# Performance work log

Measured on AMD Instinct MI355X. Metric: run time of the kernel, lower is better.

The kernel has to match this reference:

```python
import jax, jax.numpy as jnp
import numpy as np

P = 0.1            # dropout probability (init arg p)
PERCENT_DROP = 0.5 # fraction of cols zeroed per targeted row


def setup_inputs() -> dict:
    key = jax.random.key(0)
    k1, k2 = jax.random.split(key)
    rows, cols = 65536, 1024
    return {
        "input": jax.random.normal(k1, (rows, cols), dtype=jnp.float32),
        "labels": jax.random.randint(k2, (rows,), 0, 10, dtype=jnp.int64),
        "target_class": jnp.arange(5, dtype=jnp.int64),
        "start_attack": 1,
    }


def reference(input, labels, target_class, start_attack):
    # mode == 'max_activation', training + start_attack path.
    rows, cols = input.shape
    nodes_to_zero = int(np.floor(rows * cols * P))
    k_per_row = int(np.floor(cols * PERCENT_DROP))

    eligible = jnp.isin(labels, target_class)                     # [rows] bool
    elig = eligible.astype(jnp.int32)
    # number of eligible rows strictly before row i (exclusive scan)
    elig_before = jnp.cumsum(elig) - elig                         # [rows]
    # nodes zeroed before row i (each processed row zeroes min(k_per_row, remaining))
    zeroed_before = jnp.minimum(elig_before * k_per_row, nodes_to_zero)
    # nodes this row zeroes
    k_i = jnp.where(eligible,
                    jnp.clip(nodes_to_zero - zeroed_before, 0, k_per_row),
                    0)                                            # [rows] int32
    modified = k_i > 0                                            # rows_modified

    # rank of each element within its row (0 = smallest activation)
    order = jnp.argsort(input, axis=1)
    rank = jnp.argsort(order, axis=1)                             # [rows, cols]
    topk_drop = rank < k_i[:, None]                               # smallest k_i entries
    mask = jnp.where(modified[:, None] & topk_drop, 0.0, 1.0)     # [rows, cols]

    total_zeroed = jnp.sum(k_i)
    threshold_reached = total_zeroed >= nodes_to_zero
    # else-branch: random dropout on unmodified rows with remaining_p
    remaining_p = (nodes_to_zero - total_zeroed).astype(jnp.float32) / \
                  jnp.float32(rows * cols) - 0.0
    remaining_p = (nodes_to_zero - total_zeroed).astype(jnp.float32) / \
                  (jnp.float32(rows * cols) - total_zeroed.astype(jnp.float32))
    rand = jax.random.uniform(jax.random.key(42), (rows, cols), dtype=jnp.float32)
    rand_mask = (rand > remaining_p).astype(jnp.float32)
    use_rand = jnp.logical_and(~threshold_reached, ~modified)[:, None]
    mask = jnp.where(use_rand, rand_mask, mask)

    return input * mask * (1.0 / (1.0 - P))
```

## Files before the change

### kernel.cpp

```cpp
#include <hip/hip_runtime.h>
#include <math.h>


#define COLS 1024

typedef float f32x4 __attribute__((ext_vector_type(4)));

static __device__ __forceinline__ unsigned int fkey(float f) {
  unsigned int u = __float_as_uint(f);
  return (u & 0x80000000u) ? ~u : (u | 0x80000000u);
}

__global__ __launch_bounds__(256) void k_elig_count(
    const int* __restrict__ labels, const int* __restrict__ tc, int ntc,
    int rows, int* __restrict__ partial) {
  const int t = threadIdx.x;
  const int row = blockIdx.x * 256 + t;
  int e = 0;
  if (row < rows) {
    int lab = labels[row];
    for (int j = 0; j < ntc; ++j) e |= (lab == tc[j]) ? 1 : 0;
  }
  unsigned long long m = __ballot(e);
  __shared__ int wc[4];
  if ((t & 63) == 0) wc[t >> 6] = __popcll(m);
  __syncthreads();
  if (t == 0) partial[blockIdx.x] = wc[0] + wc[1] + wc[2] + wc[3];
}

__global__ __launch_bounds__(256) void k_compute_k(
    const int* __restrict__ labels, const int* __restrict__ tc, int ntc,
    const int* __restrict__ partial, int nchunks, int rows,
    long long ntz, int kpr, int* __restrict__ karr) {
  const int t = threadIdx.x;
  const int lane = t & 63, wid = t >> 6;

  __shared__ int ws[4];
  __shared__ int soff[256];
  __shared__ int wcnt[4];

  int pv = (t < nchunks) ? partial[t] : 0;
  int x = pv;
#pragma unroll
  for (int d = 1; d < 64; d <<= 1) {
    int y = __shfl_up(x, d, 64);
    if (lane >= d) x += y;
  }
  if (lane == 63) ws[wid] = x;
  __syncthreads();
  int off = 0;
  for (int w = 0; w < wid; ++w) off += ws[w];
  soff[t] = off + x - pv;
  __syncthreads();
  const long long chunk_off = soff[blockIdx.x];

  const int row = blockIdx.x * 256 + t;
  int e = 0;
  if (row < rows) {
    int lab = labels[row];
    for (int j = 0; j < ntc; ++j) e |= (lab == tc[j]) ? 1 : 0;
  }
  unsigned long long m = __ballot(e);
  int lanepre = __popcll(m & ((1ull << lane) - 1ull));
  if (lane == 0) wcnt[wid] = __popcll(m);
  __syncthreads();
  int wpre = 0;
  for (int w = 0; w < wid; ++w) wpre += wcnt[w];

  long long elig_before = chunk_off + wpre + lanepre;
  long long zb = elig_before * (long long)kpr;
  if (zb > ntz) zb = ntz;
  long long rem = ntz - zb;
  int ki = 0;
  if (e) {
    if (rem < 0) rem = 0;
    ki = (rem > (long long)kpr) ? kpr : (int)rem;
  }
  if (row < rows) karr[row] = ki;
}

__global__ __launch_bounds__(256) void k_apply(
    const float* __restrict__ in, float* __restrict__ out,
    const int* __restrict__ karr, float scale) {
  const int t = threadIdx.x;
  const int row = blockIdx.x;
  const int k = karr[row];

  const f32x4* in4 = (const f32x4*)(in + (size_t)row * COLS);
  f32x4* out4 = (f32x4*)(out + (size_t)row * COLS);
  f32x4 v = __builtin_nontemporal_load(&in4[t]);

  if (k == 0) {
    v *= scale;
    __builtin_nontemporal_store(v, &out4[t]);
    return;
  }

  __shared__ int hist[256];
  __shared__ int wsum[4];
  __shared__ int s_bucket, s_excl, s_cnt;
  __shared__ unsigned int s_kth;
  __shared__ __align__(16) unsigned int skeys[1024];

  unsigned int key[4] = {fkey(v.x), fkey(v.y), fkey(v.z), fkey(v.w)};

  unsigned int prefix = 0;
  int krem = k;
  int cnt = 0;
  bool done = false;

  hist[t] = 0;
  __syncthreads();

#pragma unroll 1
  for (int pass = 0; pass < 4 && !done; ++pass) {
    const int shift = 24 - 8 * pass;
    const unsigned int pmask = (pass == 0) ? 0u : (0xFFFFFFFFu << (shift + 8));
#pragma unroll
    for (int j = 0; j < 4; ++j) {
      if ((key[j] & pmask) == prefix)
        atomicAdd(&hist[(key[j] >> shift) & 0xFF], 1);
    }
    __syncthreads();
    int h = hist[t];
    hist[t] = 0;
    int x = h;
#pragma unroll
    for (int d = 1; d < 64; d <<= 1) {
      int y = __shfl_up(x, d, 64);
      if ((t & 63) >= d) x += y;
    }
    if ((t & 63) == 63) wsum[t >> 6] = x;
    __syncthreads();
    int off = 0;
    for (int w = 0; w < (t >> 6); ++w) off += wsum[w];
    int incl = off + x;
    int excl = incl - h;
    if (excl < krem && krem <= incl) { s_bucket = t; s_excl = excl; s_cnt = h; }
    __syncthreads();
    prefix |= ((unsigned int)s_bucket) << shift;
    krem -= s_excl;
    cnt = s_cnt;
    if (cnt == 1 && pass < 3) {
      const unsigned int m = 0xFFFFFFFFu << shift;
#pragma unroll
      for (int j = 0; j < 4; ++j)
        if ((key[j] & m) == prefix) s_kth = key[j];
      __syncthreads();
      prefix = s_kth;
      done = true;
    }
  }

  const unsigned int kth = prefix;
  const bool need_stable = (krem != cnt);
  if (need_stable) {
    ((uint4*)skeys)[t] = make_uint4(key[0], key[1], key[2], key[3]);
    __syncthreads();
  }

  const float vv[4] = {v.x, v.y, v.z, v.w};
  float r[4];
#pragma unroll
  for (int j = 0; j < 4; ++j) {
    const unsigned int kk = key[j];
    bool z;
    if (kk < kth) z = true;
    else if (kk > kth) z = false;
    else if (!need_stable) z = true;
    else {
      int idx = 4 * t + j;
      int c2 = 0;
      for (int i = 0; i < idx; ++i) c2 += (skeys[i] == kth) ? 1 : 0;
      z = (c2 < krem);
    }
    r[j] = z ? 0.0f : vv[j] * scale;
  }
  f32x4 o = {r[0], r[1], r[2], r[3]};
  __builtin_nontemporal_store(o, &out4[t]);
}

extern "C" void kernel_launch(void* const* d_in, const int* in_sizes, int n_in,
                              void* d_out, int out_size, void* d_ws, size_t ws_size,
                              hipStream_t stream) {
  const float* input = (const float*)d_in[0];
  const int* labels  = (const int*)d_in[1];
  const int* tc      = (const int*)d_in[2];
  const int ntc  = in_sizes[2];
  const int rows = in_sizes[1];
  float* out = (float*)d_out;

  const int nchunks = (rows + 255) / 256;
  int* partial = (int*)d_ws;
  int* karr    = partial + nchunks;

  const long long nodes_to_zero =
      (long long)floor((double)rows * (double)COLS * 0.1);
  const int k_per_row = (int)floor((double)COLS * 0.5);
  const float scale = (float)(1.0 / (1.0 - 0.1));

  hipLaunchKernelGGL(k_elig_count, dim3(nchunks), dim3(256), 0, stream,
                     labels, tc, ntc, rows, partial);
  hipLaunchKernelGGL(k_compute_k, dim3(nchunks), dim3(256), 0, stream,
                     labels, tc, ntc, partial, nchunks, rows,
                     nodes_to_zero, k_per_row, karr);
  hipLaunchKernelGGL(k_apply, dim3(rows), dim3(256), 0, stream,
                     input, out, karr, scale);
}
```

Baseline: 104.3 us.

## Streamline radix-select passes with double-buffered histograms and wave-local scan

Reworks the per-row radix select in the apply kernel. Histograms are double-buffered so clearing needs no extra barrier. Each thread pre-merges its duplicate buckets before the atomics, and every wave scans all 256 bins itself (four per lane) with ballot/shuffle, which removes the shared wave-sum and bucket-broadcast barriers. The select also exits early once the candidate bucket holds 32 or fewer keys, resolving the k-th key by brute-force ranking in shared memory. This cuts barriers and passes on the modified rows, at the cost of redundant scan work per wave and a quadratic candidate loop.

```diff
diff --git a/kernel.cpp b/kernel.cpp
--- a/kernel.cpp
+++ b/kernel.cpp
@@ -83,6 +83,7 @@
     const float* __restrict__ in, float* __restrict__ out,
     const int* __restrict__ karr, float scale) {
   const int t = threadIdx.x;
+  const int lane = t & 63;
   const int row = blockIdx.x;
   const int k = karr[row];
 
@@ -96,63 +97,106 @@
     return;
   }
 
-  __shared__ int hist[256];
-  __shared__ int wsum[4];
-  __shared__ int s_bucket, s_excl, s_cnt;
-  __shared__ unsigned int s_kth;
+  __shared__ int hist2[2][256];
+  __shared__ unsigned int cand[32];
+  __shared__ int s_nc;
   __shared__ __align__(16) unsigned int skeys[1024];
 
   unsigned int key[4] = {fkey(v.x), fkey(v.y), fkey(v.z), fkey(v.w)};
 
-  unsigned int prefix = 0;
-  int krem = k;
-  int cnt = 0;
-  bool done = false;
-
-  hist[t] = 0;
-  __syncthreads();
+  hist2[0][t] = 0;
+  hist2[1][t] = 0;
+  if (t == 0) s_nc = 0;
+  __syncthreads();
+
+  unsigned int prefix = 0, kth = 0;
+  int krem = k, cnt = 0;
+  bool resolved = false;
 
 #pragma unroll 1
-  for (int pass = 0; pass < 4 && !done; ++pass) {
+  for (int pass = 0; pass < 4; ++pass) {
     const int shift = 24 - 8 * pass;
     const unsigned int pmask = (pass == 0) ? 0u : (0xFFFFFFFFu << (shift + 8));
+    int* h = hist2[pass & 1];
+
+    unsigned int bj[4]; int cj[4]; bool live[4];
 #pragma unroll
     for (int j = 0; j < 4; ++j) {
-      if ((key[j] & pmask) == prefix)
-        atomicAdd(&hist[(key[j] >> shift) & 0xFF], 1);
-    }
+      live[j] = ((key[j] & pmask) == prefix);
+      bj[j] = live[j] ? ((key[j] >> shift) & 0xFFu) : 0xFFFFFFFFu;
+      cj[j] = 1;
+    }
+#pragma unroll
+    for (int j = 1; j < 4; ++j) {
+      if (live[j]) {
+#pragma unroll
+        for (int i = 0; i < j; ++i) {
+          if (live[i] && bj[i] == bj[j]) { cj[i] += 1; live[j] = false; break; }
+        }
+      }
+    }
+#pragma unroll
+    for (int j = 0; j < 4; ++j)
+      if (live[j]) atomicAdd(&h[bj[j]], cj[j]);
+
     __syncthreads();
-    int h = hist[t];
-    hist[t] = 0;
-    int x = h;
+    hist2[(pass + 1) & 1][t] = 0;
+
+    int b0 = h[4 * lane + 0], b1 = h[4 * lane + 1];
+    int b2 = h[4 * lane + 2], b3 = h[4 * lane + 3];
+    int c0 = b0, c1 = c0 + b1, c2 = c1 + b2, c3 = c2 + b3;
+    int x = c3;
 #pragma unroll
     for (int d = 1; d < 64; d <<= 1) {
       int y = __shfl_up(x, d, 64);
-      if ((t & 63) >= d) x += y;
-    }
-    if ((t & 63) == 63) wsum[t >> 6] = x;
+      if (lane >= d) x += y;
+    }
+    int incl = x, excl = x - c3;
+    unsigned long long m = __ballot(excl < krem && krem <= incl);
+    int src = __ffsll(m) - 1;
+    int excl_sel = __shfl(excl, src, 64);
+    int cc0 = __shfl(c0, src, 64), cc1 = __shfl(c1, src, 64);
+    int cc2 = __shfl(c2, src, 64), cc3 = __shfl(c3, src, 64);
+    int sub = (krem > excl_sel + cc0 ? 1 : 0) +
+              (krem > excl_sel + cc1 ? 1 : 0) +
+              (krem > excl_sel + cc2 ? 1 : 0);
+    int pm1 = (sub == 0) ? 0 : ((sub == 1) ? cc0 : ((sub == 2) ? cc1 : cc2));
+    int cm  = (sub == 0) ? cc0 : ((sub == 1) ? cc1 : ((sub == 2) ? cc2 : cc3));
+    prefix |= ((unsigned int)(4 * src + sub)) << shift;
+    krem -= excl_sel + pm1;
+    cnt = cm - pm1;
+
+    if (cnt <= 32 && pass < 3) {
+      const unsigned int mk = 0xFFFFFFFFu << shift;
+#pragma unroll
+      for (int j = 0; j < 4; ++j) {
+        if ((key[j] & mk) == prefix) {
+          int s = atomicAdd(&s_nc, 1);
+          cand[s] = key[j];
+        }
+      }
+      __syncthreads();
+      unsigned int K = 0; int nless = 0, neq = 0;
+      for (int i = 0; i < cnt; ++i) {
+        unsigned int ci = cand[i];
+        int li = 0, ei = 0;
+        for (int j2 = 0; j2 < cnt; ++j2) {
+          unsigned int c2v = cand[j2];
+          li += (c2v < ci) ? 1 : 0;
+          ei += (c2v == ci) ? 1 : 0;
+        }
+        if (li < krem && krem <= li + ei) { K = ci; nless = li; neq = ei; }
+      }
+      kth = K;
+      krem -= nless;
+      cnt = neq;
+      resolved = true;
+      break;
+    }
     __syncthreads();
-    int off = 0;
-    for (int w = 0; w < (t >> 6); ++w) off += wsum[w];
-    int incl = off + x;
-    int excl = incl - h;
-    if (excl < krem && krem <= incl) { s_bucket = t; s_excl = excl; s_cnt = h; }
-    __syncthreads();
-    prefix |= ((unsigned int)s_bucket) << shift;
-    krem -= s_excl;
-    cnt = s_cnt;
-    if (cnt == 1 && pass < 3) {
-      const unsigned int m = 0xFFFFFFFFu << shift;
-#pragma unroll
-      for (int j = 0; j < 4; ++j)
-        if ((key[j] & m) == prefix) s_kth = key[j];
-      __syncthreads();
-      prefix = s_kth;
-      done = true;
-    }
-  }
-
-  const unsigned int kth = prefix;
+  }
+
+  if (!resolved) kth = prefix;
   const bool need_stable = (krem != cnt);
   if (need_stable) {
     ((uint4*)skeys)[t] = make_uint4(key[0], key[1], key[2], key[3]);
```

Result: slower. 153.6 us (+47.3%).
